# Optimization experiments

Measured on AMD Instinct MI355X. Metric: run time of the kernel, lower is better.

## Reference

```python
import jax, jax.numpy as jnp
import numpy as np

N_EMBD = 1024
N_HEADS = 16
HEAD_DIM = N_EMBD // N_HEADS


def setup_inputs() -> dict:
    key = jax.random.key(0)
    ks = jax.random.split(key, 6)
    s = 1.0 / np.sqrt(N_EMBD)
    x = jax.random.normal(ks[0], (2, 2048, N_EMBD), dtype=jnp.float32)
    # torch Linear weights are [out, in]; y = x @ W.T
    Wk = jax.random.uniform(ks[1], (N_EMBD, N_EMBD), jnp.float32, -s, s)
    Wq = jax.random.uniform(ks[2], (N_EMBD, N_EMBD), jnp.float32, -s, s)
    Wv = jax.random.uniform(ks[3], (N_EMBD, N_EMBD), jnp.float32, -s, s)
    Wp = jax.random.uniform(ks[4], (N_EMBD, N_EMBD), jnp.float32, -s, s)
    bp = jax.random.uniform(ks[5], (N_EMBD,), jnp.float32, -s, s)
    return {"x": x, "Wq": Wq, "Wk": Wk, "Wv": Wv, "Wp": Wp, "bp": bp}


def reference(x, Wq, Wk, Wv, Wp, bp):
    B, T, C = x.shape
    H, D = N_HEADS, HEAD_DIM
    # projections (torch Linear: x @ W.T), reshape to [B, H, T, D]
    q = (x @ Wq.T).reshape(B, T, H, D).transpose(0, 2, 1, 3)
    k = (x @ Wk.T).reshape(B, T, H, D).transpose(0, 2, 1, 3)
    v = (x @ Wv.T).reshape(B, T, H, D).transpose(0, 2, 1, 3)
    # scaled causal attention, full [B,H,T,T] scores (faithful to original)
    att = jnp.einsum('bhqd,bhkd->bhqk', q, k) * (D ** -0.5)
    causal = jnp.tril(jnp.ones((T, T), dtype=bool))
    att = jnp.where(causal[None, None], att, -jnp.inf)
    att = jax.nn.softmax(att, axis=-1)
    out = jnp.einsum('bhqk,bhkd->bhqd', att, v)
    out = out.transpose(0, 2, 1, 3).reshape(B, T, C)
    return out @ Wp.T + bp
```

## Files before the change

kernel.cpp:

```cpp
#include <hip/hip_runtime.h>

typedef __bf16 bf16;
typedef __bf16 bf16x8 __attribute__((ext_vector_type(8)));
typedef float f32x4 __attribute__((ext_vector_type(4)));

typedef __attribute__((address_space(1))) const void as1_void;
typedef __attribute__((address_space(3))) void as3_void;

#define DEV __device__ __forceinline__
#define NEG_BIG (-1.0e30f)


DEV void async_load16(const void* g, void* l) {
  __builtin_amdgcn_global_load_lds((as1_void*)g, (as3_void*)l, 16, 0, 0);
}
DEV bf16x8 load8(const bf16* p) { bf16x8 v; __builtin_memcpy(&v, p, 16); return v; }
DEV void store8(bf16* p, bf16x8 v) { __builtin_memcpy(p, &v, 16); }

DEV int sniff_bf16(const unsigned short* __restrict__ xr) {
  const int lane = threadIdx.x & 63;
  const unsigned short w = xr[lane * 2];
  const int e = (w >> 7) & 0xFF;
  const bool sane = ((w & 0x7FFF) == 0) || (e >= 97 && e <= 157);
  return __popcll(__ballot(sane)) >= 48;
}

struct ConvArgs {
  const void* src[6];
  bf16* dst[6];
  int n[6];
};

__global__ __launch_bounds__(256) void convert_kernel(ConvArgs a) {
  const int isbf = sniff_bf16((const unsigned short*)a.src[0]);
  const int t = blockIdx.y;
  const int n = a.n[t];
  bf16* d = a.dst[t];
  const int stride = gridDim.x * 256 * 8;
  if (isbf) {
    const bf16* s = (const bf16*)a.src[t];
    for (int i = (blockIdx.x * 256 + threadIdx.x) * 8; i < n; i += stride)
      store8(d + i, load8(s + i));
  } else {
    const float* s = (const float*)a.src[t];
    for (int i = (blockIdx.x * 256 + threadIdx.x) * 8; i < n; i += stride) {
      float tmp[8];
      __builtin_memcpy(tmp, s + i, 32);
      bf16x8 v;
#pragma unroll
      for (int j = 0; j < 8; ++j) v[j] = (bf16)tmp[j];
      store8(d + i, v);
    }
  }
}

DEV void gemm_core_128_p(const bf16* A, const bf16* W, const int K, int m0, int n0,
                         f32x4 (&acc)[4][4]) {
  __shared__ alignas(16) bf16 As[3][128 * 32];
  __shared__ alignas(16) bf16 Bs[3][128 * 32];
  const int tid = threadIdx.x;
  const int lane = tid & 63;
  const int wid = tid >> 6;
  const int wm = (wid >> 1) << 6;
  const int wn = (wid & 1) << 6;
  const int lr = lane & 15;
  const int lg = lane >> 4;

  size_t srcA[2], srcB[2];
  int ldsoff[2];
#pragma unroll
  for (int it = 0; it < 2; ++it) {
    const int lin = it * 256 + tid;
    const int lr2 = lin >> 3, c = lin & 7;
    const int u = c ^ (lr2 & 7);
    const int r = lr2 * 2 + (u >> 2);
    const int g = u & 3;
    srcA[it] = (size_t)(m0 + r) * K + (size_t)(g * 8);
    srcB[it] = (size_t)(n0 + r) * K + (size_t)(g * 8);
    ldsoff[it] = lin * 8;
  }
  int offA[4], offB[4];
#pragma unroll
  for (int i = 0; i < 4; ++i) {
    const int r = wm + i * 16 + lr;
    const int cc = (lg | ((r & 1) << 2)) ^ ((r >> 1) & 7);
    offA[i] = (((r >> 1) << 3) | cc) * 8;
  }
#pragma unroll
  for (int j = 0; j < 4; ++j) {
    const int r = wn + j * 16 + lr;
    const int cc = (lg | ((r & 1) << 2)) ^ ((r >> 1) & 7);
    offB[j] = (((r >> 1) << 3) | cc) * 8;
  }

  const f32x4 zero = {0.f, 0.f, 0.f, 0.f};
#pragma unroll
  for (int i = 0; i < 4; ++i)
#pragma unroll
    for (int j = 0; j < 4; ++j) acc[i][j] = zero;

  const int nt = K >> 5;

  auto stage = [&](int buf, int t) {
    const size_t k0 = (size_t)(t << 5);
#pragma unroll
    for (int it = 0; it < 2; ++it) {
      async_load16(A + srcA[it] + k0, &As[buf][0] + ldsoff[it]);
      async_load16(W + srcB[it] + k0, &Bs[buf][0] + ldsoff[it]);
    }
  };

  auto compute = [&](int buf) {
    const bf16* as = &As[buf][0];
    const bf16* bs = &Bs[buf][0];
    bf16x8 af[4], bfr[4];
#pragma unroll
    for (int i = 0; i < 4; ++i) af[i] = load8(as + offA[i]);
#pragma unroll
    for (int j = 0; j < 4; ++j) bfr[j] = load8(bs + offB[j]);
    __builtin_amdgcn_s_setprio(1);
#pragma unroll
    for (int i = 0; i < 4; ++i)
#pragma unroll
      for (int j = 0; j < 4; ++j)
        acc[i][j] = __builtin_amdgcn_mfma_f32_16x16x32_bf16(af[i], bfr[j], acc[i][j], 0, 0, 0);
    __builtin_amdgcn_s_setprio(0);
  };

  stage(0, 0);
  stage(1, 1);
  int b0 = 0, b1 = 1, b2 = 2;
  for (int t = 0; t < nt; ++t) {
    if (t + 1 < nt) asm volatile("s_waitcnt vmcnt(4)" ::: "memory");
    else            asm volatile("s_waitcnt vmcnt(0)" ::: "memory");
    __builtin_amdgcn_s_barrier();
    if (t + 2 < nt) stage(b2, t + 2);
    compute(b0);
    const int tmp = b0; b0 = b1; b1 = b2; b2 = tmp;
  }
}

DEV size_t frag_idx(int row, int col) {
  return ((size_t)(((col >> 5) * 4 + ((row >> 4) & 3)) * 64 + ((col >> 3) & 3) * 16 + (row & 15)) << 3)
         | (size_t)(col & 7);
}

__global__ __launch_bounds__(256) void qkv_proj_kernel(
    const bf16* __restrict__ x, const bf16* __restrict__ Wq,
    const bf16* __restrict__ Wk, const bf16* __restrict__ Wv,
    bf16* __restrict__ q_ws, bf16* __restrict__ k_ws, bf16* __restrict__ vt_ws) {
  const int L = blockIdx.x;
  const int xcd = L & 7;
  const int i2 = L >> 3;
  const int m0 = (xcd * 4 + (i2 & 3)) << 7;
  const int rest = i2 >> 2;
  const int n0 = (rest & 7) << 7;
  const int mode = rest >> 3;
  const bf16* W = (mode == 0) ? Wq : (mode == 1) ? Wk : Wv;
  f32x4 acc[4][4];
  gemm_core_128_p(x, W, 1024, m0, n0, acc);

  const int tid = threadIdx.x;
  const int lane = tid & 63, wid = tid >> 6;
  const int wm = (wid >> 1) << 6, wn = (wid & 1) << 6;
  const int lr = lane & 15, lg = lane >> 4;
  bf16* out = (mode == 0) ? q_ws : (mode == 1) ? k_ws : vt_ws;
#pragma unroll
  for (int i = 0; i < 4; ++i) {
#pragma unroll
    for (int r = 0; r < 4; ++r) {
      const int m = m0 + wm + i * 16 + lg * 4 + r;
      const int b = m >> 11, t = m & 2047;
#pragma unroll
      for (int j = 0; j < 4; ++j) {
        const int n = n0 + wn + j * 16 + lr;
        const int h = n >> 6, d = n & 63;
        const float v = acc[i][j][r];
        const size_t base = ((size_t)(b * 16 + h) << 17) + ((size_t)(t >> 6) << 12);
        const size_t idx = base + ((mode < 2) ? frag_idx(t & 63, d) : frag_idx(d, t & 63));
        out[idx] = (bf16)v;
      }
    }
  }
}

__global__ __launch_bounds__(256, 2) void attn_kernel(
    const bf16* __restrict__ q_ws, const bf16* __restrict__ k_ws,
    const bf16* __restrict__ vt_ws, bf16* __restrict__ a_ws) {
  const int L = blockIdx.x;
  const int xcd = L & 7;
  const int bh = xcd * 4 + ((L >> 3) & 3);
  const int qt = 31 - (L >> 5);
  const int tid = threadIdx.x;
  const int lane = tid & 63, w = tid >> 6;
  const int lr = lane & 15, lg = lane >> 4;
  const int fo = lg * 16 + lr;

  __shared__ alignas(16) bf16 Ps[4][16 * 72];
  bf16* ps = &Ps[w][0];

  const size_t hb = (size_t)bh << 17;
  const int b = bh >> 4, h = bh & 15;
  const f32x4 zero = {0.f, 0.f, 0.f, 0.f};

  const size_t qtb = hb + ((size_t)qt << 12);

  bf16x8 aq[2];
#pragma unroll
  for (int c2 = 0; c2 < 2; ++c2)
    aq[c2] = load8(q_ws + qtb + (size_t)(((c2 * 4 + w) * 64 + fo) << 3));

  f32x4 o_acc[4];
#pragma unroll
  for (int j = 0; j < 4; ++j) o_acc[j] = zero;
  float lsum[4] = {0.f, 0.f, 0.f, 0.f};

  auto load_k = [&](bf16x8 (&bk)[4][2], int kt) {
    const size_t ktb = hb + ((size_t)kt << 12);
#pragma unroll
    for (int j = 0; j < 4; ++j)
#pragma unroll
      for (int c2 = 0; c2 < 2; ++c2)
        bk[j][c2] = load8(k_ws + ktb + (size_t)(((c2 * 4 + j) * 64 + fo) << 3));
  };

  auto step = [&](const bf16x8 (&bk)[4][2], int kt, bool diag) {
    const size_t ktb = hb + ((size_t)kt << 12);
    bf16x8 bv[4][2];
#pragma unroll
    for (int j = 0; j < 4; ++j)
#pragma unroll
      for (int c2 = 0; c2 < 2; ++c2)
        bv[j][c2] = load8(vt_ws + ktb + (size_t)(((c2 * 4 + j) * 64 + fo) << 3));

    f32x4 s[4];
#pragma unroll
    for (int j = 0; j < 4; ++j) {
      s[j] = __builtin_amdgcn_mfma_f32_16x16x32_bf16(aq[0], bk[j][0], zero, 0, 0, 0);
      s[j] = __builtin_amdgcn_mfma_f32_16x16x32_bf16(aq[1], bk[j][1], s[j], 0, 0, 0);
    }
    float p[4][4];
#pragma unroll
    for (int j = 0; j < 4; ++j) {
#pragma unroll
      for (int r = 0; r < 4; ++r) {
        float v = s[j][r] * 0.125f;
        if (diag && (j * 16 + lr) > (w * 16 + lg * 4 + r)) v = NEG_BIG;
        p[j][r] = __expf(v);
      }
    }
#pragma unroll
    for (int r = 0; r < 4; ++r)
      lsum[r] += (p[0][r] + p[1][r]) + (p[2][r] + p[3][r]);
#pragma unroll
    for (int j = 0; j < 4; ++j)
#pragma unroll
      for (int r = 0; r < 4; ++r)
        ps[(lg * 4 + r) * 72 + j * 16 + lr] = (bf16)p[j][r];
#pragma unroll
    for (int c2 = 0; c2 < 2; ++c2) {
      const bf16x8 ap = load8(ps + lr * 72 + c2 * 32 + lg * 8);
#pragma unroll
      for (int j = 0; j < 4; ++j)
        o_acc[j] = __builtin_amdgcn_mfma_f32_16x16x32_bf16(ap, bv[j][c2], o_acc[j], 0, 0, 0);
    }
  };

  bf16x8 bkA[4][2], bkB[4][2];
  const int n = qt;
  load_k(bkA, qt);
  if (n > 0) load_k(bkB, 0);
  step(bkA, qt, true);
  int kt = 0;
  while (kt + 1 < n) {
    load_k(bkA, kt + 1);
    step(bkB, kt, false);
    if (kt + 2 < n) load_k(bkB, kt + 2);
    step(bkA, kt + 1, false);
    kt += 2;
  }
  if (kt < n) step(bkB, kt, false);

  float l_i[4];
#pragma unroll
  for (int r = 0; r < 4; ++r) {
    float v = lsum[r];
#pragma unroll
    for (int off = 1; off < 16; off <<= 1) v += __shfl_xor(v, off, 64);
    l_i[r] = v;
  }

#pragma unroll
  for (int r = 0; r < 4; ++r) {
    const int t = qt * 64 + w * 16 + lg * 4 + r;
    const float inv = 1.f / l_i[r];
#pragma unroll
    for (int j = 0; j < 4; ++j) {
      const size_t idx = (((size_t)(b * 2048 + t)) << 10) | (size_t)(h * 64 + j * 16 + lr);
      a_ws[idx] = (bf16)(o_acc[j][r] * inv);
    }
  }
}

__global__ __launch_bounds__(256) void out_proj_kernel(
    const bf16* __restrict__ A, const bf16* __restrict__ Wp,
    const bf16* __restrict__ bp, void* __restrict__ out,
    const unsigned short* __restrict__ xraw) {
  const int L = blockIdx.x;
  const int xcd = L & 7;
  const int i2 = L >> 3;
  const int m0 = (xcd * 4 + (i2 & 3)) << 7;
  const int n0 = (i2 >> 2) << 7;
  f32x4 acc[4][4];
  gemm_core_128_p(A, Wp, 1024, m0, n0, acc);

  const int tid = threadIdx.x;
  const int lane = tid & 63, wid = tid >> 6;
  const int wm = (wid >> 1) << 6, wn = (wid & 1) << 6;
  const int lr = lane & 15, lg = lane >> 4;
  const int isbf = sniff_bf16(xraw);
#pragma unroll
  for (int i = 0; i < 4; ++i) {
#pragma unroll
    for (int r = 0; r < 4; ++r) {
      const int m = m0 + wm + i * 16 + lg * 4 + r;
#pragma unroll
      for (int j = 0; j < 4; ++j) {
        const int n = n0 + wn + j * 16 + lr;
        const float v = acc[i][j][r] + (float)bp[n];
        const size_t idx = ((size_t)m << 10) | (size_t)n;
        if (isbf) ((bf16*)out)[idx] = (bf16)v;
        else      ((float*)out)[idx] = v;
      }
    }
  }
}

extern "C" void kernel_launch(void* const* d_in, const int* in_sizes, int n_in,
                              void* d_out, int out_size, void* d_ws, size_t ws_size,
                              hipStream_t stream) {
  (void)in_sizes; (void)n_in; (void)out_size;
  if (ws_size < (50u << 20)) return;

  char* ws = (char*)d_ws;
  bf16* q_ws  = (bf16*)(ws);
  bf16* k_ws  = (bf16*)(ws + (8u << 20));
  bf16* vt_ws = (bf16*)(ws + (16u << 20));
  bf16* a_ws  = (bf16*)(ws + (24u << 20));
  bf16* xc    = (bf16*)(ws + (32u << 20));
  bf16* Wqc   = (bf16*)(ws + (40u << 20));
  bf16* Wkc   = (bf16*)(ws + (42u << 20));
  bf16* Wvc   = (bf16*)(ws + (44u << 20));
  bf16* Wpc   = (bf16*)(ws + (46u << 20));
  bf16* bpc   = (bf16*)(ws + (48u << 20));

  ConvArgs ca;
  ca.src[0] = d_in[0]; ca.dst[0] = xc;  ca.n[0] = 4096 * 1024;
  ca.src[1] = d_in[1]; ca.dst[1] = Wqc; ca.n[1] = 1024 * 1024;
  ca.src[2] = d_in[2]; ca.dst[2] = Wkc; ca.n[2] = 1024 * 1024;
  ca.src[3] = d_in[3]; ca.dst[3] = Wvc; ca.n[3] = 1024 * 1024;
  ca.src[4] = d_in[4]; ca.dst[4] = Wpc; ca.n[4] = 1024 * 1024;
  ca.src[5] = d_in[5]; ca.dst[5] = bpc; ca.n[5] = 1024;
  convert_kernel<<<dim3(512, 6), 256, 0, stream>>>(ca);

  qkv_proj_kernel<<<768, 256, 0, stream>>>(xc, Wqc, Wkc, Wvc, q_ws, k_ws, vt_ws);
  attn_kernel<<<1024, 256, 0, stream>>>(q_ws, k_ws, vt_ws, a_ws);
  out_proj_kernel<<<256, 256, 0, stream>>>(a_ws, Wpc, bpc, d_out,
                                           (const unsigned short*)d_in[0]);
}
```

Baseline: 183.5 us.

## Stage K/V tiles through triple-buffered LDS with async global-to-LDS loads

```diff
diff --git a/kernel.cpp b/kernel.cpp
--- a/kernel.cpp
+++ b/kernel.cpp
@@ -196,6 +196,8 @@
   const int lr = lane & 15, lg = lane >> 4;
   const int fo = lg * 16 + lr;
 
+  __shared__ alignas(16) bf16 Ks[3][4096];
+  __shared__ alignas(16) bf16 Vs[3][4096];
   __shared__ alignas(16) bf16 Ps[4][16 * 72];
   bf16* ps = &Ps[w][0];
 
@@ -204,6 +206,8 @@
   const f32x4 zero = {0.f, 0.f, 0.f, 0.f};
 
   const size_t qtb = hb + ((size_t)qt << 12);
+  const bf16* kbase = k_ws + hb;
+  const bf16* vbase = vt_ws + hb;
 
   bf16x8 aq[2];
 #pragma unroll
@@ -215,30 +219,34 @@
   for (int j = 0; j < 4; ++j) o_acc[j] = zero;
   float lsum[4] = {0.f, 0.f, 0.f, 0.f};
 
-  auto load_k = [&](bf16x8 (&bk)[4][2], int kt) {
-    const size_t ktb = hb + ((size_t)kt << 12);
-#pragma unroll
-    for (int j = 0; j < 4; ++j)
-#pragma unroll
-      for (int c2 = 0; c2 < 2; ++c2)
-        bk[j][c2] = load8(k_ws + ktb + (size_t)(((c2 * 4 + j) * 64 + fo) << 3));
+  const int nt = qt + 1;
+  auto ktof = [&](int s) { return (s == 0) ? qt : (s - 1); };
+
+  auto stage = [&](int buf, int s) {
+    const int kt = ktof(s);
+    const bf16* kg = kbase + ((size_t)kt << 12);
+    const bf16* vg = vbase + ((size_t)kt << 12);
+#pragma unroll
+    for (int it = 0; it < 2; ++it) {
+      const int lin = it * 256 + tid;
+      async_load16(kg + lin * 8, &Ks[buf][0] + lin * 8);
+      async_load16(vg + lin * 8, &Vs[buf][0] + lin * 8);
+    }
   };
 
-  auto step = [&](const bf16x8 (&bk)[4][2], int kt, bool diag) {
-    const size_t ktb = hb + ((size_t)kt << 12);
-    bf16x8 bv[4][2];
-#pragma unroll
-    for (int j = 0; j < 4; ++j)
-#pragma unroll
-      for (int c2 = 0; c2 < 2; ++c2)
-        bv[j][c2] = load8(vt_ws + ktb + (size_t)(((c2 * 4 + j) * 64 + fo) << 3));
-
+  auto step = [&](int buf, bool diag) {
+    const bf16* ks = &Ks[buf][0];
+    const bf16* vs = &Vs[buf][0];
     f32x4 s[4];
+    __builtin_amdgcn_s_setprio(1);
 #pragma unroll
     for (int j = 0; j < 4; ++j) {
-      s[j] = __builtin_amdgcn_mfma_f32_16x16x32_bf16(aq[0], bk[j][0], zero, 0, 0, 0);
-      s[j] = __builtin_amdgcn_mfma_f32_16x16x32_bf16(aq[1], bk[j][1], s[j], 0, 0, 0);
-    }
+      s[j] = __builtin_amdgcn_mfma_f32_16x16x32_bf16(
+          aq[0], load8(ks + (size_t)(((0 * 4 + j) * 64 + fo) << 3)), zero, 0, 0, 0);
+      s[j] = __builtin_amdgcn_mfma_f32_16x16x32_bf16(
+          aq[1], load8(ks + (size_t)(((1 * 4 + j) * 64 + fo) << 3)), s[j], 0, 0, 0);
+    }
+    __builtin_amdgcn_s_setprio(0);
     float p[4][4];
 #pragma unroll
     for (int j = 0; j < 4; ++j) {
@@ -257,29 +265,29 @@
 #pragma unroll
       for (int r = 0; r < 4; ++r)
         ps[(lg * 4 + r) * 72 + j * 16 + lr] = (bf16)p[j][r];
+    __builtin_amdgcn_s_setprio(1);
 #pragma unroll
     for (int c2 = 0; c2 < 2; ++c2) {
       const bf16x8 ap = load8(ps + lr * 72 + c2 * 32 + lg * 8);
 #pragma unroll
       for (int j = 0; j < 4; ++j)
-        o_acc[j] = __builtin_amdgcn_mfma_f32_16x16x32_bf16(ap, bv[j][c2], o_acc[j], 0, 0, 0);
-    }
+        o_acc[j] = __builtin_amdgcn_mfma_f32_16x16x32_bf16(
+            ap, load8(vs + (size_t)(((c2 * 4 + j) * 64 + fo) << 3)), o_acc[j], 0, 0, 0);
+    }
+    __builtin_amdgcn_s_setprio(0);
   };
 
-  bf16x8 bkA[4][2], bkB[4][2];
-  const int n = qt;
-  load_k(bkA, qt);
-  if (n > 0) load_k(bkB, 0);
-  step(bkA, qt, true);
-  int kt = 0;
-  while (kt + 1 < n) {
-    load_k(bkA, kt + 1);
-    step(bkB, kt, false);
-    if (kt + 2 < n) load_k(bkB, kt + 2);
-    step(bkA, kt + 1, false);
-    kt += 2;
-  }
-  if (kt < n) step(bkB, kt, false);
+  stage(0, 0);
+  if (nt > 1) stage(1, 1);
+  int b0 = 0, b1 = 1, b2 = 2;
+  for (int t = 0; t < nt; ++t) {
+    if (t + 1 < nt) asm volatile("s_waitcnt vmcnt(4)" ::: "memory");
+    else            asm volatile("s_waitcnt vmcnt(0)" ::: "memory");
+    __builtin_amdgcn_s_barrier();
+    if (t + 2 < nt) stage(b2, t + 2);
+    step(b0, t == 0);
+    const int tmp = b0; b0 = b1; b1 = b2; b2 = tmp;
+  }
 
   float l_i[4];
 #pragma unroll
```

After: 184.9 us. About the same (+0.8%).
